# Kernel tuning notes

Hardware: AMD Instinct MI355X
Metric: run time of the kernel (lower is better)

Reference implementation:

```python
import jax, jax.numpy as jnp
import numpy as np


def setup_inputs() -> dict:
    key = jax.random.key(0)
    k1, k2 = jax.random.split(key)
    bsz, beam_size = 64, 8
    R = bsz * beam_size  # 512 rows
    step = 511
    seq_len = step + 1
    vocab = 50257
    n = 3
    tokens = jax.random.randint(k1, (R, seq_len), 0, 100, dtype=jnp.int64)
    lprobs = jax.random.normal(k2, (R, vocab), dtype=jnp.float32)
    return {
        "tokens": tokens,
        "lprobs": lprobs,
        "bsz": bsz,
        "step": step,
        "beam_size": beam_size,
        "no_repeat_ngram_size": n,
    }


def reference(tokens, lprobs, bsz, step, beam_size, no_repeat_ngram_size):
    # tokens: (bsz*beam, seq_len) int; lprobs: (bsz*beam, vocab) float
    n = no_repeat_ngram_size
    R, V = lprobs.shape
    num_starts = step - n + 2  # number of historical n-gram start positions
    if num_starts < 1:
        return lprobs
    starts = jnp.arange(num_starts)
    # windows of the first (n-1) tokens of each historical n-gram: (R, S, n-1)
    win_idx = starts[:, None] + jnp.arange(n - 1)
    windows = tokens[:, win_idx]
    # current (n-1)-token suffix ending at `step`: (R, n-1)
    suffix = tokens[:, step - n + 2 : step + 1]
    match = jnp.all(windows == suffix[:, None, :], axis=-1)  # (R, S)
    banned = tokens[:, starts + n - 1]  # token completing each matched n-gram
    rows = jnp.arange(R)[:, None]
    ban_mask = jnp.zeros((R, V), dtype=bool).at[rows, banned].max(match)
    return jnp.where(ban_mask, -jnp.inf, lprobs)
```

## Files before the change

### kernel.cpp

```cpp
#include <hip/hip_runtime.h>


#define BAN_VALUE (-3.3895313892515355e+38f)

__global__ void ban_kernel(const int* __restrict__ tokens,
                           const int* __restrict__ step_p,
                           const int* __restrict__ n_p,
                           float* __restrict__ out,
                           int seq_len, int V) {
    const int row  = blockIdx.x;
    const int step = *step_p;
    const int n    = *n_p;
    const int num_starts = step - n + 2;
    if (num_starts < 1) return;

    bool is64 = true;
    for (int k = 1; k < 64; k += 2) {
        if (tokens[k] != 0) { is64 = false; break; }
    }
    const long long* t64 = (const long long*)tokens;
    const int*       t32 = tokens;
    const long base = (long)row * seq_len;

    #define TOK(i) (is64 ? (int)t64[base + (i)] : t32[base + (i)])

    const int suf0 = step - n + 2;

    for (int s = threadIdx.x; s < num_starts; s += blockDim.x) {
        bool match = true;
        for (int j = 0; j < n - 1; ++j) {
            if (TOK(s + j) != TOK(suf0 + j)) { match = false; break; }
        }
        if (match) {
            int banned = TOK(s + n - 1);
            if (banned < 0) banned = 0;
            if (banned >= V) banned = V - 1;
            out[(long)row * V + banned] = BAN_VALUE;
        }
    }
    #undef TOK
}

extern "C" void kernel_launch(void* const* d_in, const int* in_sizes, int n_in,
                              void* d_out, int out_size, void* d_ws, size_t ws_size,
                              hipStream_t stream) {
    const int* tokens = (const int*)d_in[0];
    const void* lprobs = d_in[1];
    const int* step_p = (const int*)d_in[3];
    const int* n_p    = (const int*)d_in[5];
    float* out = (float*)d_out;

    const int R = 512;
    const int seq_len = in_sizes[0] / R;
    const int V = out_size / R;

    hipMemcpyAsync(out, lprobs, (size_t)out_size * sizeof(float),
                   hipMemcpyDeviceToDevice, stream);

    ban_kernel<<<R, 256, 0, stream>>>(tokens, step_p, n_p, out, seq_len, V);
}
```

Baseline: 194.6 us.

## Fuse lprobs copy and n-gram banning into one vectorized kernel

Replaces the device-to-device memcpy plus separate per-row ban kernel with one kernel. Each block copies a 4096-float chunk with float4 loads and stores. Before copying, the block rescans the token history of the rows its chunk overlaps and applies any banned positions in registers. This removes the second pass over the output and a separate launch. In exchange, every block redoes the n-gram match for one or two rows. Bans are capped at 128 per chunk in shared memory, and any ban beyond that cap would be silently dropped.

```diff
diff --git a/kernel.cpp b/kernel.cpp
--- a/kernel.cpp
+++ b/kernel.cpp
@@ -2,50 +2,100 @@
 
 
 #define BAN_VALUE (-3.3895313892515355e+38f)
+#define F4_PER_THREAD 4
+#define BLOCK_THREADS 256
+#define CHUNK_F4 (BLOCK_THREADS * F4_PER_THREAD)
 
-__global__ void ban_kernel(const int* __restrict__ tokens,
-                           const int* __restrict__ step_p,
-                           const int* __restrict__ n_p,
-                           float* __restrict__ out,
-                           int seq_len, int V) {
-    const int row  = blockIdx.x;
+__global__ __launch_bounds__(BLOCK_THREADS)
+void fused_kernel(const float4* __restrict__ in, float4* __restrict__ out,
+                  int n4,
+                  const int* __restrict__ tokens,
+                  const int* __restrict__ step_p,
+                  const int* __restrict__ n_p,
+                  int seq_len, int V, int R) {
+    __shared__ int s_count;
+    __shared__ int s_ban[128];
+
+    const int tid = threadIdx.x;
+    const long chunk0 = (long)blockIdx.x * CHUNK_F4;
+    if (tid == 0) s_count = 0;
+    __syncthreads();
+
     const int step = *step_p;
     const int n    = *n_p;
     const int num_starts = step - n + 2;
-    if (num_starts < 1) return;
 
-    bool is64 = true;
-    for (int k = 1; k < 64; k += 2) {
-        if (tokens[k] != 0) { is64 = false; break; }
-    }
-    const long long* t64 = (const long long*)tokens;
-    const int*       t32 = tokens;
-    const long base = (long)row * seq_len;
+    if (num_starts >= 1) {
+        bool is64 = true;
+        for (int k = 1; k < 64; k += 2) {
+            if (tokens[k] != 0) { is64 = false; break; }
+        }
+        const long long* t64 = (const long long*)tokens;
 
-    #define TOK(i) (is64 ? (int)t64[base + (i)] : t32[base + (i)])
+        const long f_lo = chunk0 * 4;
+        long f_hi = (chunk0 + CHUNK_F4) * 4;
+        const long f_end = (long)n4 * 4;
+        if (f_hi > f_end) f_hi = f_end;
 
-    const int suf0 = step - n + 2;
+        int row0 = (int)(f_lo / V);
+        int row1 = (int)((f_hi - 1) / V);
+        if (row1 >= R) row1 = R - 1;
+        const int suf0 = step - n + 2;
 
-    for (int s = threadIdx.x; s < num_starts; s += blockDim.x) {
-        bool match = true;
-        for (int j = 0; j < n - 1; ++j) {
-            if (TOK(s + j) != TOK(suf0 + j)) { match = false; break; }
-        }
-        if (match) {
-            int banned = TOK(s + n - 1);
-            if (banned < 0) banned = 0;
-            if (banned >= V) banned = V - 1;
-            out[(long)row * V + banned] = BAN_VALUE;
+        for (int r = row0; r <= row1; ++r) {
+            const long base = (long)r * seq_len;
+            for (int s = tid; s < num_starts; s += BLOCK_THREADS) {
+                bool match = true;
+                for (int j = 0; j < n - 1; ++j) {
+                    const int a = is64 ? (int)t64[base + s + j]
+                                       : tokens[base + s + j];
+                    const int b = is64 ? (int)t64[base + suf0 + j]
+                                       : tokens[base + suf0 + j];
+                    if (a != b) { match = false; break; }
+                }
+                if (match) {
+                    int banned = is64 ? (int)t64[base + s + n - 1]
+                                      : tokens[base + s + n - 1];
+                    if (banned < 0) banned = 0;
+                    if (banned >= V) banned = V - 1;
+                    const long f = (long)r * V + banned;
+                    if (f >= f_lo && f < f_hi) {
+                        const int slot = atomicAdd(&s_count, 1);
+                        if (slot < 128) s_ban[slot] = (int)(f - f_lo);
+                    }
+                }
+            }
         }
     }
-    #undef TOK
+    __syncthreads();
+    int cnt = s_count;
+    if (cnt > 128) cnt = 128;
+
+    #pragma unroll
+    for (int u = 0; u < F4_PER_THREAD; ++u) {
+        const long i4 = chunk0 + (long)u * BLOCK_THREADS + tid;
+        if (i4 < n4) {
+            float4 v = in[i4];
+            if (cnt > 0) {
+                const int local0 = (int)((i4 - chunk0) * 4);
+                for (int b = 0; b < cnt; ++b) {
+                    const int d = s_ban[b] - local0;
+                    if (d == 0) v.x = BAN_VALUE;
+                    else if (d == 1) v.y = BAN_VALUE;
+                    else if (d == 2) v.z = BAN_VALUE;
+                    else if (d == 3) v.w = BAN_VALUE;
+                }
+            }
+            out[i4] = v;
+        }
+    }
 }
 
 extern "C" void kernel_launch(void* const* d_in, const int* in_sizes, int n_in,
                               void* d_out, int out_size, void* d_ws, size_t ws_size,
                               hipStream_t stream) {
-    const int* tokens = (const int*)d_in[0];
-    const void* lprobs = d_in[1];
+    const int*   tokens = (const int*)d_in[0];
+    const float* lprobs = (const float*)d_in[1];
     const int* step_p = (const int*)d_in[3];
     const int* n_p    = (const int*)d_in[5];
     float* out = (float*)d_out;
@@ -54,8 +104,9 @@
     const int seq_len = in_sizes[0] / R;
     const int V = out_size / R;
 
-    hipMemcpyAsync(out, lprobs, (size_t)out_size * sizeof(float),
-                   hipMemcpyDeviceToDevice, stream);
-
-    ban_kernel<<<R, 256, 0, stream>>>(tokens, step_p, n_p, out, seq_len, V);
+    const int n4 = out_size / 4;
+    const int blocks = (n4 + CHUNK_F4 - 1) / CHUNK_F4;
+    fused_kernel<<<blocks, BLOCK_THREADS, 0, stream>>>(
+        (const float4*)lprobs, (float4*)out, n4,
+        tokens, step_p, n_p, seq_len, V, R);
 }
```

Result: no change. 198.4 us (+1.9%).
